# Performance work log

Measured on AMD Instinct MI355X. Metric: run time of the kernel, lower is better.

## Reference

```python
import jax, jax.numpy as jnp
import numpy as np

N_NODES = 100000
N_EDGES = 1600000
IN_C, HID_C, OUT_C = 128, 64, 32


def setup_inputs() -> dict:
    key = jax.random.key(0)
    k1, k2, k3, k4 = jax.random.split(key, 4)
    x = jax.random.normal(k1, (N_NODES, IN_C), dtype=jnp.float32)
    edge_index = jax.random.randint(k2, (2, N_EDGES), 0, N_NODES, dtype=jnp.int64)
    # glorot-style init for GCN linear weights
    W1 = jax.random.normal(k3, (IN_C, HID_C), dtype=jnp.float32) * (2.0 / (IN_C + HID_C)) ** 0.5
    b1 = jnp.zeros((HID_C,), dtype=jnp.float32)
    W2 = jax.random.normal(k4, (HID_C, OUT_C), dtype=jnp.float32) * (2.0 / (HID_C + OUT_C)) ** 0.5
    b2 = jnp.zeros((OUT_C,), dtype=jnp.float32)
    return {"x": x, "edge_index": edge_index, "W1": W1, "b1": b1, "W2": W2, "b2": b2}


def _gcn_conv(h, row, col, norm, n, b):
    # gather transformed source features, scale by symmetric norm, scatter-add to targets
    msg = h[row] * norm[:, None]            # [E+N, C]
    return jax.ops.segment_sum(msg, col, num_segments=n) + b


def reference(x, edge_index, W1, b1, W2, b2):
    n = x.shape[0]
    loops = jnp.arange(n, dtype=edge_index.dtype)
    row = jnp.concatenate([edge_index[0], loops])   # sources (with self-loops)
    col = jnp.concatenate([edge_index[1], loops])   # targets
    deg = jax.ops.segment_sum(jnp.ones_like(col, dtype=x.dtype), col, num_segments=n)
    dinv = jnp.where(deg > 0, jax.lax.rsqrt(deg), 0.0)
    norm = dinv[row] * dinv[col]                    # D^{-1/2} A_hat D^{-1/2}
    h = jax.nn.relu(_gcn_conv(x @ W1, row, col, norm, n, b1))
    out = _gcn_conv(h @ W2, row, col, norm, n, b2)
    return out
```

## Files before the change

### kernel.cpp

```cpp
#include <hip/hip_runtime.h>

#define IN_C 128
#define HID_C 64
#define OUT_C 32
#define NBLK 512
#define NBUCK 512
#define CAP 5120

typedef unsigned int uint;

__device__ __forceinline__ uint bf16pair(float a, float b) {
  uint ua = __float_as_uint(a), ub = __float_as_uint(b);
  ua = (ua + 0x7FFFu + ((ua >> 16) & 1u)) >> 16;
  ub = (ub + 0x7FFFu + ((ub >> 16) & 1u)) >> 16;
  return ua | (ub << 16);
}

__device__ __forceinline__ void acc8(float* acc, uint4 q) {
  acc[0] += __uint_as_float(q.x << 16);
  acc[1] += __uint_as_float(q.x & 0xFFFF0000u);
  acc[2] += __uint_as_float(q.y << 16);
  acc[3] += __uint_as_float(q.y & 0xFFFF0000u);
  acc[4] += __uint_as_float(q.z << 16);
  acc[5] += __uint_as_float(q.z & 0xFFFF0000u);
  acc[6] += __uint_as_float(q.w << 16);
  acc[7] += __uint_as_float(q.w & 0xFFFF0000u);
}


__global__ void __launch_bounds__(256) scatter_reserve_kernel(
    const int* __restrict__ row, const int* __restrict__ col,
    int* __restrict__ gcur, int* __restrict__ ebuf, int e, int epb) {
  __shared__ int hist[NBUCK];
  __shared__ int cur[NBUCK];
  int t = threadIdx.x, b = blockIdx.x;
  for (int i = t; i < NBUCK; i += 256) hist[i] = 0;
  __syncthreads();
  int s = b * epb, en = min(e, s + epb);
  for (int i = s + t; i < en; i += 256) atomicAdd(&hist[col[i] >> 8], 1);
  __syncthreads();
  for (int i = t; i < NBUCK; i += 256) {
    int h = hist[i];
    int base = h ? atomicAdd(&gcur[i], h) : 0;
    cur[i] = CAP * i + base;
  }
  __syncthreads();
  for (int i = s + t; i < en; i += 256) {
    int c = col[i], r = row[i];
    int bk = c >> 8;
    int p = atomicAdd(&cur[bk], 1);
    if (p < CAP * bk + CAP) ebuf[p] = r | ((c & 255) << 17);
  }
}

__global__ void __launch_bounds__(256) csr_kernel(const int* __restrict__ ebuf,
                                                  const int* __restrict__ gcur,
                                                  int* __restrict__ offS, int* __restrict__ offE,
                                                  int* __restrict__ srt, float* __restrict__ dinv,
                                                  int n) {
  __shared__ int cnt[256];
  __shared__ int base[256];
  int t = threadIdx.x, b = blockIdx.x;
  int es = b * CAP;
  int ec = min(gcur[b], CAP);
  cnt[t] = 0;
  __syncthreads();
  for (int i = t; i < ec; i += 256) atomicAdd(&cnt[(ebuf[es + i] >> 17) & 255], 1);
  __syncthreads();
  int v = cnt[t];
  base[t] = v;
  __syncthreads();
  for (int d = 1; d < 256; d <<= 1) {
    int a = (t >= d) ? base[t - d] : 0;
    __syncthreads();
    base[t] += a;
    __syncthreads();
  }
  int gstart = es + base[t] - v;
  int node = b * 256 + t;
  if (node < n) {
    offS[node] = gstart;
    offE[node] = gstart + v;
    dinv[node] = rsqrtf((float)(v + 1));
  }
  base[t] = gstart;
  __syncthreads();
  for (int i = t; i < ec; i += 256) {
    int pv = ebuf[es + i];
    int pos = atomicAdd(&base[(pv >> 17) & 255], 1);
    srt[pos] = pv & 0x1FFFF;
  }
}


__global__ void gemm1_kernel(const float* __restrict__ x, const float* __restrict__ W1,
                             const float* __restrict__ dinv, unsigned short* __restrict__ xw1b,
                             int n) {
  __shared__ float w1s[IN_C * HID_C];
  __shared__ float xs[16 * IN_C];
  int tid = threadIdx.x;
  for (int i = tid; i < IN_C * HID_C; i += 256) w1s[i] = W1[i];
  int row0 = blockIdx.x * 16;
  const float4* x4 = (const float4*)(x + (size_t)row0 * IN_C);
  float4* xs4 = (float4*)xs;
  for (int i = tid; i < 16 * IN_C / 4; i += 256) {
    int grow = row0 + i / (IN_C / 4);
    if (grow < n) xs4[i] = x4[i];
  }
  __syncthreads();
  int r = tid >> 4;
  int c0 = (tid & 15) * 4;
  int row = row0 + r;
  if (row >= n) return;
  float a0 = 0.f, a1 = 0.f, a2 = 0.f, a3 = 0.f;
  const float* xr = xs + r * IN_C;
  for (int k = 0; k < IN_C; ++k) {
    float xv = xr[k];
    const float* w = w1s + k * HID_C + c0;
    a0 += xv * w[0];
    a1 += xv * w[1];
    a2 += xv * w[2];
    a3 += xv * w[3];
  }
  float dv = dinv[row];
  uint2 o = make_uint2(bf16pair(a0 * dv, a1 * dv), bf16pair(a2 * dv, a3 * dv));
  ((uint2*)(xw1b + (size_t)row * HID_C))[tid & 15] = o;
}

__global__ void __launch_bounds__(256) gather1_gemm2_kernel(
    const int* __restrict__ offS, const int* __restrict__ offE, const int* __restrict__ srt,
    const float* __restrict__ dinv, const unsigned short* __restrict__ xw1b,
    const float* __restrict__ b1, const float* __restrict__ W2,
    unsigned short* __restrict__ hw2b, int n) {
  __shared__ float w2s[HID_C * OUT_C];
  __shared__ float hs[32][HID_C];
  int t = threadIdx.x;
  for (int i = t; i < HID_C * OUT_C; i += 256) w2s[i] = W2[i];
  int g = t >> 3, fl = t & 7;
  int c = blockIdx.x * 32 + g;
  if (c < n) {
    int js = offS[c], je = offE[c];
    float acc[8] = {0.f, 0.f, 0.f, 0.f, 0.f, 0.f, 0.f, 0.f};
    float acc2[8] = {0.f, 0.f, 0.f, 0.f, 0.f, 0.f, 0.f, 0.f};
    int j = js;
    for (; j + 3 < je; j += 4) {
      int r0 = __builtin_nontemporal_load(srt + j);
      int r1 = __builtin_nontemporal_load(srt + j + 1);
      int r2 = __builtin_nontemporal_load(srt + j + 2);
      int r3 = __builtin_nontemporal_load(srt + j + 3);
      uint4 q0 = ((const uint4*)(xw1b + (size_t)r0 * HID_C))[fl];
      uint4 q1 = ((const uint4*)(xw1b + (size_t)r1 * HID_C))[fl];
      uint4 q2 = ((const uint4*)(xw1b + (size_t)r2 * HID_C))[fl];
      uint4 q3 = ((const uint4*)(xw1b + (size_t)r3 * HID_C))[fl];
      acc8(acc, q0); acc8(acc2, q1); acc8(acc, q2); acc8(acc2, q3);
    }
    for (; j < je; ++j) {
      int r = __builtin_nontemporal_load(srt + j);
      acc8(acc, ((const uint4*)(xw1b + (size_t)r * HID_C))[fl]);
    }
    acc8(acc, ((const uint4*)(xw1b + (size_t)c * HID_C))[fl]);
    float dv = dinv[c];
    const float4* b1v = (const float4*)b1;
    float4 blo = b1v[fl * 2], bhi = b1v[fl * 2 + 1];
    float h0 = (acc[0] + acc2[0]) * dv + blo.x;
    float h1 = (acc[1] + acc2[1]) * dv + blo.y;
    float h2 = (acc[2] + acc2[2]) * dv + blo.z;
    float h3 = (acc[3] + acc2[3]) * dv + blo.w;
    float h4 = (acc[4] + acc2[4]) * dv + bhi.x;
    float h5 = (acc[5] + acc2[5]) * dv + bhi.y;
    float h6 = (acc[6] + acc2[6]) * dv + bhi.z;
    float h7 = (acc[7] + acc2[7]) * dv + bhi.w;
    float4 lo = {h0 > 0.f ? h0 : 0.f, h1 > 0.f ? h1 : 0.f,
                 h2 > 0.f ? h2 : 0.f, h3 > 0.f ? h3 : 0.f};
    float4 hi = {h4 > 0.f ? h4 : 0.f, h5 > 0.f ? h5 : 0.f,
                 h6 > 0.f ? h6 : 0.f, h7 > 0.f ? h7 : 0.f};
    ((float4*)hs[g])[fl * 2] = lo;
    ((float4*)hs[g])[fl * 2 + 1] = hi;
  }
  __syncthreads();
  for (int task = t; task < 32 * (OUT_C / 2); task += 256) {
    int nl = task >> 4, pr = task & 15;
    int c2 = blockIdx.x * 32 + nl;
    if (c2 < n) {
      float s0 = 0.f, s1 = 0.f;
      const float* hr = hs[nl];
#pragma unroll
      for (int k = 0; k < HID_C; ++k) {
        float hv = hr[k];
        s0 += hv * w2s[k * OUT_C + pr * 2];
        s1 += hv * w2s[k * OUT_C + pr * 2 + 1];
      }
      float dv2 = dinv[c2];
      ((uint*)(hw2b + (size_t)c2 * OUT_C))[pr] = bf16pair(s0 * dv2, s1 * dv2);
    }
  }
}

__global__ void __launch_bounds__(256) gather2_kernel(
    const int* __restrict__ offS, const int* __restrict__ offE, const int* __restrict__ srt,
    const float* __restrict__ dinv, const unsigned short* __restrict__ hw2b,
    const float* __restrict__ b2, float* __restrict__ out, int n) {
  int t = threadIdx.x;
  int g = t >> 2, fl = t & 3;
  int c = blockIdx.x * 64 + g;
  if (c >= n) return;
  int js = offS[c], je = offE[c];
  float acc[8] = {0.f, 0.f, 0.f, 0.f, 0.f, 0.f, 0.f, 0.f};
  float acc2[8] = {0.f, 0.f, 0.f, 0.f, 0.f, 0.f, 0.f, 0.f};
  int j = js;
  for (; j + 3 < je; j += 4) {
    int r0 = __builtin_nontemporal_load(srt + j);
    int r1 = __builtin_nontemporal_load(srt + j + 1);
    int r2 = __builtin_nontemporal_load(srt + j + 2);
    int r3 = __builtin_nontemporal_load(srt + j + 3);
    uint4 q0 = ((const uint4*)(hw2b + (size_t)r0 * OUT_C))[fl];
    uint4 q1 = ((const uint4*)(hw2b + (size_t)r1 * OUT_C))[fl];
    uint4 q2 = ((const uint4*)(hw2b + (size_t)r2 * OUT_C))[fl];
    uint4 q3 = ((const uint4*)(hw2b + (size_t)r3 * OUT_C))[fl];
    acc8(acc, q0); acc8(acc2, q1); acc8(acc, q2); acc8(acc2, q3);
  }
  for (; j < je; ++j) {
    int r = __builtin_nontemporal_load(srt + j);
    acc8(acc, ((const uint4*)(hw2b + (size_t)r * OUT_C))[fl]);
  }
  acc8(acc, ((const uint4*)(hw2b + (size_t)c * OUT_C))[fl]);
  float dv = dinv[c];
  const float4* b2v = (const float4*)b2;
  float4 blo = b2v[fl * 2], bhi = b2v[fl * 2 + 1];
  float4 olo = {(acc[0] + acc2[0]) * dv + blo.x, (acc[1] + acc2[1]) * dv + blo.y,
                (acc[2] + acc2[2]) * dv + blo.z, (acc[3] + acc2[3]) * dv + blo.w};
  float4 ohi = {(acc[4] + acc2[4]) * dv + bhi.x, (acc[5] + acc2[5]) * dv + bhi.y,
                (acc[6] + acc2[6]) * dv + bhi.z, (acc[7] + acc2[7]) * dv + bhi.w};
  ((float4*)(out + (size_t)c * OUT_C))[fl * 2] = olo;
  ((float4*)(out + (size_t)c * OUT_C))[fl * 2 + 1] = ohi;
}

extern "C" void kernel_launch(void* const* d_in, const int* in_sizes, int n_in,
                              void* d_out, int out_size, void* d_ws, size_t ws_size,
                              hipStream_t stream) {
  const float* x  = (const float*)d_in[0];
  const int*   ei = (const int*)d_in[1];
  const float* W1 = (const float*)d_in[2];
  const float* b1 = (const float*)d_in[3];
  const float* W2 = (const float*)d_in[4];
  const float* b2 = (const float*)d_in[5];
  float* out = (float*)d_out;

  int n = in_sizes[0] / IN_C;
  int e = in_sizes[1] / 2;
  const int* row = ei;
  const int* col = ei + e;

  float* dinv = (float*)d_ws;
  int*   offS = (int*)(dinv + n);
  int*   offE = offS + n;
  int*   gcur = offE + n;
  int*   srt  = gcur + NBUCK;
  unsigned short* xw1b = (unsigned short*)(srt + (size_t)NBUCK * CAP);
  int*   ebuf = (int*)xw1b;
  unsigned short* hw2b = xw1b + (size_t)n * HID_C;

  int epb = (e + NBLK - 1) / NBLK;
  int nbuckets = (n + 255) / 256;

  hipMemsetAsync(gcur, 0, NBUCK * sizeof(int), stream);
  hipLaunchKernelGGL(scatter_reserve_kernel, dim3(NBLK), dim3(256), 0, stream,
                     row, col, gcur, ebuf, e, epb);
  hipLaunchKernelGGL(csr_kernel, dim3(nbuckets), dim3(256), 0, stream,
                     ebuf, gcur, offS, offE, srt, dinv, n);
  hipLaunchKernelGGL(gemm1_kernel, dim3((n + 15) / 16), dim3(256), 0, stream,
                     x, W1, dinv, xw1b, n);
  hipLaunchKernelGGL(gather1_gemm2_kernel, dim3((n + 31) / 32), dim3(256), 0, stream,
                     offS, offE, srt, dinv, xw1b, b1, W2, hw2b, n);
  hipLaunchKernelGGL(gather2_kernel, dim3((n + 63) / 64), dim3(256), 0, stream,
                     offS, offE, srt, dinv, hw2b, b2, out, n);
}
```

Baseline: 253.7 us.

## Replace scalar first GEMM with split-bf16 MFMA kernel

Replaces the FP32 scalar-FMA x@W1 kernel with a matrix-core kernel built on bf16 16x16x32 MFMA. To keep close to fp32 accuracy, x and W1 are each split into hi and lo bf16 parts and three MFMA products are summed. A small one-block kernel pre-transposes and splits W1 into workspace. The cost is an extra tiny launch and element-wise (non-vectorized) bf16 output stores, against a large cut in ALU work for a GEMM that was compute-heavy on shared memory.

```diff
diff --git a/kernel.cpp b/kernel.cpp
--- a/kernel.cpp
+++ b/kernel.cpp
@@ -8,12 +8,20 @@
 #define CAP 5120
 
 typedef unsigned int uint;
+typedef unsigned short ushort;
+typedef __attribute__((ext_vector_type(8))) short bf16x8;
+typedef __attribute__((ext_vector_type(4))) float f32x4;
 
 __device__ __forceinline__ uint bf16pair(float a, float b) {
   uint ua = __float_as_uint(a), ub = __float_as_uint(b);
   ua = (ua + 0x7FFFu + ((ua >> 16) & 1u)) >> 16;
   ub = (ub + 0x7FFFu + ((ub >> 16) & 1u)) >> 16;
   return ua | (ub << 16);
+}
+
+__device__ __forceinline__ uint bf16one(float a) {
+  uint u = __float_as_uint(a);
+  return (u + 0x7FFFu + ((u >> 16) & 1u)) >> 16;
 }
 
 __device__ __forceinline__ void acc8(float* acc, uint4 q) {
@@ -93,45 +101,96 @@
 }
 
 
-__global__ void gemm1_kernel(const float* __restrict__ x, const float* __restrict__ W1,
-                             const float* __restrict__ dinv, unsigned short* __restrict__ xw1b,
-                             int n) {
-  __shared__ float w1s[IN_C * HID_C];
-  __shared__ float xs[16 * IN_C];
-  int tid = threadIdx.x;
-  for (int i = tid; i < IN_C * HID_C; i += 256) w1s[i] = W1[i];
-  int row0 = blockIdx.x * 16;
-  const float4* x4 = (const float4*)(x + (size_t)row0 * IN_C);
-  float4* xs4 = (float4*)xs;
-  for (int i = tid; i < 16 * IN_C / 4; i += 256) {
-    int grow = row0 + i / (IN_C / 4);
-    if (grow < n) xs4[i] = x4[i];
-  }
-  __syncthreads();
-  int r = tid >> 4;
-  int c0 = (tid & 15) * 4;
-  int row = row0 + r;
-  if (row >= n) return;
-  float a0 = 0.f, a1 = 0.f, a2 = 0.f, a3 = 0.f;
-  const float* xr = xs + r * IN_C;
-  for (int k = 0; k < IN_C; ++k) {
-    float xv = xr[k];
-    const float* w = w1s + k * HID_C + c0;
-    a0 += xv * w[0];
-    a1 += xv * w[1];
-    a2 += xv * w[2];
-    a3 += xv * w[3];
-  }
-  float dv = dinv[row];
-  uint2 o = make_uint2(bf16pair(a0 * dv, a1 * dv), bf16pair(a2 * dv, a3 * dv));
-  ((uint2*)(xw1b + (size_t)row * HID_C))[tid & 15] = o;
+__global__ void __launch_bounds__(256) prep_w1t_kernel(const float* __restrict__ W1,
+                                                       ushort* __restrict__ w1t_hi,
+                                                       ushort* __restrict__ w1t_lo) {
+  int t = threadIdx.x;
+  for (int i = t; i < HID_C * IN_C; i += 256) {
+    int c = i >> 7, k = i & 127;
+    float v = W1[k * HID_C + c];
+    uint h = bf16one(v);
+    float lo = v - __uint_as_float(h << 16);
+    w1t_hi[i] = (ushort)h;
+    w1t_lo[i] = (ushort)bf16one(lo);
+  }
+}
+
+#define APAD 136
+__global__ void __launch_bounds__(256) gemm1_mfma_kernel(
+    const float* __restrict__ x, const ushort* __restrict__ w1t_hi,
+    const ushort* __restrict__ w1t_lo, const float* __restrict__ dinv,
+    ushort* __restrict__ xw1b, int n) {
+  __shared__ ushort xs_hi[64 * APAD];
+  __shared__ ushort xs_lo[64 * APAD];
+  __shared__ float dinv_s[64];
+  int t = threadIdx.x;
+  int row0 = blockIdx.x * 64;
+  if (t < 64) {
+    int rr = row0 + t;
+    dinv_s[t] = rr < n ? dinv[rr] : 0.f;
+  }
+  for (int task = t; task < 64 * 16; task += 256) {
+    int r = task >> 4, kc = task & 15;
+    int grow = row0 + r;
+    uint4 hq = {0u, 0u, 0u, 0u}, lq = {0u, 0u, 0u, 0u};
+    if (grow < n) {
+      const float* xp = x + (size_t)grow * IN_C + kc * 8;
+      float4 v0 = *(const float4*)xp;
+      float4 v1 = *(const float4*)(xp + 4);
+      float vv[8] = {v0.x, v0.y, v0.z, v0.w, v1.x, v1.y, v1.z, v1.w};
+      uint hu[8];
+      float lf[8];
+#pragma unroll
+      for (int i = 0; i < 8; ++i) {
+        hu[i] = bf16one(vv[i]);
+        lf[i] = vv[i] - __uint_as_float(hu[i] << 16);
+      }
+      hq = make_uint4(hu[0] | (hu[1] << 16), hu[2] | (hu[3] << 16),
+                      hu[4] | (hu[5] << 16), hu[6] | (hu[7] << 16));
+      lq = make_uint4(bf16pair(lf[0], lf[1]), bf16pair(lf[2], lf[3]),
+                      bf16pair(lf[4], lf[5]), bf16pair(lf[6], lf[7]));
+    }
+    *(uint4*)(xs_hi + r * APAD + kc * 8) = hq;
+    *(uint4*)(xs_lo + r * APAD + kc * 8) = lq;
+  }
+  __syncthreads();
+  int wv = t >> 6, lane = t & 63, m = lane & 15, q = lane >> 4;
+  f32x4 acc[4];
+#pragma unroll
+  for (int ct = 0; ct < 4; ++ct) acc[ct] = (f32x4){0.f, 0.f, 0.f, 0.f};
+  const ushort* ah_p = xs_hi + (wv * 16 + m) * APAD + q * 8;
+  const ushort* al_p = xs_lo + (wv * 16 + m) * APAD + q * 8;
+#pragma unroll
+  for (int kb = 0; kb < 4; ++kb) {
+    bf16x8 ah = *(const bf16x8*)(ah_p + kb * 32);
+    bf16x8 al = *(const bf16x8*)(al_p + kb * 32);
+#pragma unroll
+    for (int ct = 0; ct < 4; ++ct) {
+      const ushort* bp = w1t_hi + (ct * 16 + m) * IN_C + kb * 32 + q * 8;
+      bf16x8 bh = *(const bf16x8*)bp;
+      bf16x8 bl = *(const bf16x8*)(bp + (size_t)(w1t_lo - w1t_hi));
+      acc[ct] = __builtin_amdgcn_mfma_f32_16x16x32_bf16(ah, bh, acc[ct], 0, 0, 0);
+      acc[ct] = __builtin_amdgcn_mfma_f32_16x16x32_bf16(al, bh, acc[ct], 0, 0, 0);
+      acc[ct] = __builtin_amdgcn_mfma_f32_16x16x32_bf16(ah, bl, acc[ct], 0, 0, 0);
+    }
+  }
+#pragma unroll
+  for (int ct = 0; ct < 4; ++ct) {
+#pragma unroll
+    for (int rg = 0; rg < 4; ++rg) {
+      int lr = wv * 16 + q * 4 + rg;
+      int grow = row0 + lr;
+      if (grow < n)
+        xw1b[(size_t)grow * HID_C + ct * 16 + m] = (ushort)bf16one(acc[ct][rg] * dinv_s[lr]);
+    }
+  }
 }
 
 __global__ void __launch_bounds__(256) gather1_gemm2_kernel(
     const int* __restrict__ offS, const int* __restrict__ offE, const int* __restrict__ srt,
-    const float* __restrict__ dinv, const unsigned short* __restrict__ xw1b,
+    const float* __restrict__ dinv, const ushort* __restrict__ xw1b,
     const float* __restrict__ b1, const float* __restrict__ W2,
-    unsigned short* __restrict__ hw2b, int n) {
+    ushort* __restrict__ hw2b, int n) {
   __shared__ float w2s[HID_C * OUT_C];
   __shared__ float hs[32][HID_C];
   int t = threadIdx.x;
@@ -198,7 +257,7 @@
 
 __global__ void __launch_bounds__(256) gather2_kernel(
     const int* __restrict__ offS, const int* __restrict__ offE, const int* __restrict__ srt,
-    const float* __restrict__ dinv, const unsigned short* __restrict__ hw2b,
+    const float* __restrict__ dinv, const ushort* __restrict__ hw2b,
     const float* __restrict__ b2, float* __restrict__ out, int n) {
   int t = threadIdx.x;
   int g = t >> 2, fl = t & 3;
@@ -256,9 +315,11 @@
   int*   offE = offS + n;
   int*   gcur = offE + n;
   int*   srt  = gcur + NBUCK;
-  unsigned short* xw1b = (unsigned short*)(srt + (size_t)NBUCK * CAP);
+  ushort* xw1b = (ushort*)(srt + (size_t)NBUCK * CAP);
   int*   ebuf = (int*)xw1b;
-  unsigned short* hw2b = xw1b + (size_t)n * HID_C;
+  ushort* hw2b = xw1b + (size_t)n * HID_C;
+  ushort* w1t_hi = hw2b + (size_t)n * OUT_C;
+  ushort* w1t_lo = w1t_hi + HID_C * IN_C;
 
   int epb = (e + NBLK - 1) / NBLK;
   int nbuckets = (n + 255) / 256;
@@ -268,8 +329,9 @@
                      row, col, gcur, ebuf, e, epb);
   hipLaunchKernelGGL(csr_kernel, dim3(nbuckets), dim3(256), 0, stream,
                      ebuf, gcur, offS, offE, srt, dinv, n);
-  hipLaunchKernelGGL(gemm1_kernel, dim3((n + 15) / 16), dim3(256), 0, stream,
-                     x, W1, dinv, xw1b, n);
+  hipLaunchKernelGGL(prep_w1t_kernel, dim3(1), dim3(256), 0, stream, W1, w1t_hi, w1t_lo);
+  hipLaunchKernelGGL(gemm1_mfma_kernel, dim3((n + 63) / 64), dim3(256), 0, stream,
+                     x, w1t_hi, w1t_lo, dinv, xw1b, n);
   hipLaunchKernelGGL(gather1_gemm2_kernel, dim3((n + 31) / 32), dim3(256), 0, stream,
                      offS, offE, srt, dinv, xw1b, b1, W2, hw2b, n);
   hipLaunchKernelGGL(gather2_kernel, dim3((n + 63) / 64), dim3(256), 0, stream,
```

New measurement: 249.0 us. Within noise of the previous version (-1.9%).
